# Kernel tuning notes

Measured on AMD Instinct MI355X. Metric: run time of the kernel, lower is better.

Reference implementation:

```python
import jax, jax.numpy as jnp
import numpy as np

B, S, D = 4, 2048, 1024
H = 16
HD = D // H  # head_dim = 64


def setup_inputs() -> dict:
    key = jax.random.key(0)
    ks = jax.random.split(key, 8)
    scale = 1.0 / np.sqrt(D)
    return {
        "X_Q": jax.random.normal(ks[0], (B, S, D), dtype=jnp.float32),
        "X_KV": jax.random.normal(ks[1], (B, S, D), dtype=jnp.float32),
        # q_proj: Linear(D, D), weights stored as (in, out)
        "q_w": jax.random.normal(ks[2], (D, D), dtype=jnp.float32) * scale,
        "q_b": jax.random.normal(ks[3], (D,), dtype=jnp.float32) * scale,
        # kv_proj: Linear(D, 2*D)
        "kv_w": jax.random.normal(ks[4], (D, 2 * D), dtype=jnp.float32) * scale,
        "kv_b": jax.random.normal(ks[5], (2 * D,), dtype=jnp.float32) * scale,
        # out_proj: Linear(D, D) (query_dim == input_dim)
        "out_w": jax.random.normal(ks[6], (D, D), dtype=jnp.float32) * scale,
        "out_b": jax.random.normal(ks[7], (D,), dtype=jnp.float32) * scale,
    }


def reference(X_Q, X_KV, q_w, q_b, kv_w, kv_b, out_w, out_b):
    # projections
    q = X_Q @ q_w + q_b                      # [b, s, D]
    kv = X_KV @ kv_w + kv_b                  # [b, l, 2D]
    k, v = jnp.split(kv, 2, axis=-1)         # each [b, l, D]

    def split_heads(t):
        b, m, _ = t.shape
        return t.reshape(b, m, H, HD).transpose(0, 2, 1, 3)  # [b, h, m, d]

    q, k, v = split_heads(q), split_heads(k), split_heads(v)

    # standard attention: full SxL scores (non-flash path)
    scores = jnp.einsum("bhsd,bhld->bhsl", q, k) / np.sqrt(HD)
    attn = jax.nn.softmax(scores, axis=-1)   # dropout_p = 0 -> identity
    out = jnp.einsum("bhsl,bhld->bhsd", attn, v)

    # merge heads: [b, h, s, d] -> [b, s, h*d]
    out = out.transpose(0, 2, 1, 3).reshape(B, S, D)
    return out @ out_w + out_b
```

## Files before the change

kernel.cpp:

```cpp
#include <hip/hip_runtime.h>
#include <hip/hip_bf16.h>
#include <math.h>

#define B_  4
#define S_  2048
#define D_  1024
#define H_  16
#define HD_ 64

typedef __bf16 bf16;
typedef __bf16 bf16x4 __attribute__((ext_vector_type(4)));
typedef __bf16 bf16x8 __attribute__((ext_vector_type(8)));
typedef float  floatx4 __attribute__((ext_vector_type(4)));
typedef unsigned short ushort8 __attribute__((ext_vector_type(8)));

#define QSCALE 0.18033688011112042f

__device__ __forceinline__ void async_load16(const bf16* g, bf16* l) {
  __builtin_amdgcn_global_load_lds(
      (const __attribute__((address_space(1))) void*)g,
      (__attribute__((address_space(3))) void*)l, 16, 0, 0);
}

__global__ __launch_bounds__(256) void cast_f32_bf16(
    const float* __restrict__ in, bf16* __restrict__ out, int n) {
  int i = (blockIdx.x * blockDim.x + threadIdx.x) * 4;
  if (i >= n) return;
  float4 v = *reinterpret_cast<const float4*>(in + i);
  bf16x4 o;
  o[0] = (bf16)v.x; o[1] = (bf16)v.y; o[2] = (bf16)v.z; o[3] = (bf16)v.w;
  *reinterpret_cast<bf16x4*>(out + i) = o;
}

__global__ __launch_bounds__(256) void transcast(
    const float* __restrict__ in, bf16* __restrict__ out, int K, int N) {
  __shared__ float tile[32][33];
  int k0 = blockIdx.y * 32, n0 = blockIdx.x * 32;
  int tx = threadIdx.x, ty = threadIdx.y;
  #pragma unroll
  for (int i = ty; i < 32; i += 8)
    tile[i][tx] = in[(size_t)(k0 + i) * N + n0 + tx];
  __syncthreads();
  #pragma unroll
  for (int i = ty; i < 32; i += 8)
    out[(size_t)(n0 + i) * K + k0 + tx] = (bf16)tile[tx][i];
}

template <int MODE>
__global__ __launch_bounds__(256) void gemm_bt(
    const bf16* __restrict__ A, const bf16* __restrict__ Bt,
    const float* __restrict__ bias, void* __restrict__ out,
    int M, int N, int K) {
  __shared__ bf16 As[128][64];
  __shared__ bf16 Bs[128][64];

  const int tid  = threadIdx.x;
  const int m0   = blockIdx.y * 128;
  const int n0   = blockIdx.x * 128;
  const int w    = tid >> 6;
  const int lane = tid & 63;
  const int lr   = lane & 15;
  const int lq   = lane >> 4;
  const int wm   = (w >> 1) * 64;
  const int wn   = (w & 1) * 64;

  const int srow = lane >> 3;
  const int sg   = (lane & 7) ^ srow;
  const bf16* aptr = A  + (size_t)(m0 + 32 * w + srow) * K + 8 * sg;
  const bf16* bptr = Bt + (size_t)(n0 + 32 * w + srow) * K + 8 * sg;

  floatx4 acc[4][4];
  #pragma unroll
  for (int i = 0; i < 4; i++)
    #pragma unroll
    for (int j = 0; j < 4; j++)
      acc[i][j] = floatx4{0.f, 0.f, 0.f, 0.f};

  for (int k0 = 0; k0 < K; k0 += 64) {
    __syncthreads();
    #pragma unroll
    for (int p = 0; p < 4; p++) {
      async_load16(aptr + (size_t)8 * p * K + k0, &As[32 * w + 8 * p][0]);
      async_load16(bptr + (size_t)8 * p * K + k0, &Bs[32 * w + 8 * p][0]);
    }
    __syncthreads();
    #pragma unroll
    for (int kc = 0; kc < 2; kc++) {
      const int sw = 8 * ((kc * 4 + lq) ^ (lr & 7));
      bf16x8 af[4], bfv[4];
      #pragma unroll
      for (int t = 0; t < 4; t++)
        af[t] = *reinterpret_cast<const bf16x8*>(&As[wm + 16 * t + lr][sw]);
      #pragma unroll
      for (int t = 0; t < 4; t++)
        bfv[t] = *reinterpret_cast<const bf16x8*>(&Bs[wn + 16 * t + lr][sw]);
      #pragma unroll
      for (int i = 0; i < 4; i++)
        #pragma unroll
        for (int j = 0; j < 4; j++)
          acc[i][j] = __builtin_amdgcn_mfma_f32_16x16x32_bf16(af[i], bfv[j], acc[i][j], 0, 0, 0);
    }
  }

  #pragma unroll
  for (int i = 0; i < 4; i++) {
    int row_base = m0 + wm + 16 * i + lq * 4;
    #pragma unroll
    for (int j = 0; j < 4; j++) {
      int col = n0 + wn + 16 * j + lr;
      float bv = bias[col];
      if (MODE == 2 && col >= 1024) {
        int b = row_base >> 11, s0 = row_base & 2047;
        int c = col - 1024, h = c >> 6, d = c & 63;
        bf16* Vt = (bf16*)out + (size_t)B_ * H_ * S_ * HD_;
        bf16x4 pk;
        #pragma unroll
        for (int r = 0; r < 4; r++) pk[r] = (bf16)(acc[i][j][r] + bv);
        *reinterpret_cast<bf16x4*>(
            &Vt[(((size_t)b * H_ + h) * HD_ + d) * S_ + s0]) = pk;
        continue;
      }
      #pragma unroll
      for (int r = 0; r < 4; r++) {
        int row = row_base + r;
        float v = acc[i][j][r] + bv;
        if (MODE == 0) {
          ((float*)out)[(size_t)row * N + col] = v;
        } else if (MODE == 1) {
          int b = row >> 11, s = row & 2047;
          int h = col >> 6, d = col & 63;
          ((bf16*)out)[(((size_t)b * H_ + h) * S_ + s) * HD_ + d] =
              (bf16)(v * QSCALE);
        } else {
          int b = row >> 11, s = row & 2047;
          int h = col >> 6, d = col & 63;
          ((bf16*)out)[(((size_t)b * H_ + h) * S_ + s) * HD_ + d] = (bf16)v;
        }
      }
    }
  }
}

__global__ __launch_bounds__(256, 4) void attn_kernel(
    const bf16* __restrict__ Q, const bf16* __restrict__ Kb,
    const bf16* __restrict__ Vt, bf16* __restrict__ out) {
  __shared__ bf16 smem[128 * 64 + 64 * 64 + 64 * 64];
  bf16 (*qs)[64]  = (bf16(*)[64])smem;
  bf16 (*ks)[64]  = (bf16(*)[64])(smem + 128 * 64);
  bf16 (*vts)[64] = (bf16(*)[64])(smem + 128 * 64 + 64 * 64);

  const int tid  = threadIdx.x;
  const int w    = tid >> 6;
  const int lane = tid & 63;
  const int lr   = lane & 15;
  const int lq   = lane >> 4;
  const int q0   = blockIdx.x * 128;
  const int bh   = blockIdx.y;
  const size_t base = (size_t)bh * S_ * HD_;

  bf16 (*pw)[64] = (bf16(*)[64])(smem + w * 2048);

  const int srow = lane >> 3;
  const int sg   = (lane & 7) ^ srow;

  const bf16* qsrc = Q  + base + (size_t)(q0 + 32 * w + srow) * HD_ + 8 * sg;
  #pragma unroll
  for (int p = 0; p < 4; p++)
    async_load16(qsrc + (size_t)8 * p * HD_, &qs[32 * w + 8 * p][0]);

  const bf16* kptr = Kb + base + (size_t)(16 * w + srow) * HD_ + 8 * sg;
  const bf16* vptr = Vt + base + (size_t)(16 * w + srow) * S_  + 8 * sg;

  #pragma unroll
  for (int p = 0; p < 2; p++) {
    async_load16(kptr + (size_t)8 * p * HD_, &ks[16 * w + 8 * p][0]);
    async_load16(vptr + (size_t)8 * p * S_,  &vts[16 * w + 8 * p][0]);
  }
  __syncthreads();

  const int sw0 = 8 * ((0 + lq) ^ (lr & 7));
  const int sw1 = 8 * ((4 + lq) ^ (lr & 7));
  bf16x8 bq[2][2];
  #pragma unroll
  for (int grp = 0; grp < 2; grp++) {
    bq[grp][0] = *reinterpret_cast<const bf16x8*>(&qs[32 * w + 16 * grp + lr][sw0]);
    bq[grp][1] = *reinterpret_cast<const bf16x8*>(&qs[32 * w + 16 * grp + lr][sw1]);
  }

  float l_i[2] = {0.f, 0.f};
  floatx4 o_acc[2][4];
  #pragma unroll
  for (int grp = 0; grp < 2; grp++)
    #pragma unroll
    for (int t = 0; t < 4; t++) o_acc[grp][t] = floatx4{0.f, 0.f, 0.f, 0.f};

  const int NIT = S_ / 64;
  for (int it = 0; it < NIT; it++) {
    floatx4 sc[2][4];
    #pragma unroll
    for (int grp = 0; grp < 2; grp++)
      #pragma unroll
      for (int t = 0; t < 4; t++) sc[grp][t] = floatx4{0.f, 0.f, 0.f, 0.f};
    #pragma unroll
    for (int kc = 0; kc < 2; kc++) {
      const int sw = kc ? sw1 : sw0;
      #pragma unroll
      for (int t = 0; t < 4; t++) {
        bf16x8 ak = *reinterpret_cast<const bf16x8*>(&ks[16 * t + lr][sw]);
        sc[0][t] = __builtin_amdgcn_mfma_f32_16x16x32_bf16(ak, bq[0][kc], sc[0][t], 0, 0, 0);
        sc[1][t] = __builtin_amdgcn_mfma_f32_16x16x32_bf16(ak, bq[1][kc], sc[1][t], 0, 0, 0);
      }
    }

    #pragma unroll
    for (int grp = 0; grp < 2; grp++) {
      float lsum = 0.f;
      #pragma unroll
      for (int t = 0; t < 4; t++) {
        bf16x4 pk;
        #pragma unroll
        for (int r = 0; r < 4; r++) {
          float p = __builtin_amdgcn_exp2f(sc[grp][t][r]);
          lsum += p;
          pk[r] = (bf16)p;
        }
        int col = 8 * ((2 * t + (lq >> 1)) ^ (lr & 7)) + 4 * (lq & 1);
        *reinterpret_cast<bf16x4*>(&pw[16 * grp + lr][col]) = pk;
      }
      l_i[grp] += lsum;
    }
    __builtin_amdgcn_wave_barrier();

    #pragma unroll
    for (int kc = 0; kc < 2; kc++) {
      const int sw = kc ? sw1 : sw0;
      bf16x8 bp0 = *reinterpret_cast<const bf16x8*>(&pw[lr][sw]);
      bf16x8 bp1 = *reinterpret_cast<const bf16x8*>(&pw[16 + lr][sw]);
      #pragma unroll
      for (int t = 0; t < 4; t++) {
        bf16x8 av = *reinterpret_cast<const bf16x8*>(&vts[16 * t + lr][sw]);
        o_acc[0][t] = __builtin_amdgcn_mfma_f32_16x16x32_bf16(av, bp0, o_acc[0][t], 0, 0, 0);
        o_acc[1][t] = __builtin_amdgcn_mfma_f32_16x16x32_bf16(av, bp1, o_acc[1][t], 0, 0, 0);
      }
    }

    if (it + 1 < NIT) {
      __syncthreads();
      const int l0n = (it + 1) * 64;
      #pragma unroll
      for (int p = 0; p < 2; p++) {
        async_load16(kptr + (size_t)(l0n + 8 * p) * HD_, &ks[16 * w + 8 * p][0]);
        async_load16(vptr + (size_t)8 * p * S_ + l0n,    &vts[16 * w + 8 * p][0]);
      }
      __syncthreads();
    }
  }

  #pragma unroll
  for (int grp = 0; grp < 2; grp++) {
    l_i[grp] += __shfl_xor(l_i[grp], 16, 64);
    l_i[grp] += __shfl_xor(l_i[grp], 32, 64);
  }

  const int b = bh >> 4, h = bh & 15;
  #pragma unroll
  for (int grp = 0; grp < 2; grp++) {
    const float inv = 1.0f / l_i[grp];
    const int qrow = q0 + 32 * w + 16 * grp + lr;
    bf16* orow = out + ((size_t)b * S_ + qrow) * D_ + h * HD_;
    #pragma unroll
    for (int t = 0; t < 4; t++) {
      bf16x4 pk;
      #pragma unroll
      for (int r = 0; r < 4; r++) pk[r] = (bf16)(o_acc[grp][t][r] * inv);
      *reinterpret_cast<bf16x4*>(&orow[16 * t + lq * 4]) = pk;
    }
  }
}

extern "C" void kernel_launch(void* const* d_in, const int* in_sizes, int n_in,
                              void* d_out, int out_size, void* d_ws, size_t ws_size,
                              hipStream_t stream) {
  const float* X_Q   = (const float*)d_in[0];
  const float* X_KV  = (const float*)d_in[1];
  const float* q_w   = (const float*)d_in[2];
  const float* q_b   = (const float*)d_in[3];
  const float* kv_w  = (const float*)d_in[4];
  const float* kv_b  = (const float*)d_in[5];
  const float* out_w = (const float*)d_in[6];
  const float* out_b = (const float*)d_in[7];
  float* out = (float*)d_out;

  char* ws = (char*)d_ws;
  const size_t MB = 1024 * 1024;
  bf16* Xq   = (bf16*)(ws + 0);
  bf16* Xkv  = (bf16*)(ws + 16 * MB);
  bf16* Qb   = (bf16*)(ws + 32 * MB);
  bf16* Kb   = (bf16*)(ws + 48 * MB);
  bf16* qwT  = (bf16*)(ws + 80 * MB);
  bf16* kvwT = (bf16*)(ws + 82 * MB);
  bf16* owT  = (bf16*)(ws + 86 * MB);
  bf16* Vt   = Kb + (size_t)B_ * H_ * S_ * HD_;
  bf16* attn = Xq;

  const int nX = B_ * S_ * D_;

  cast_f32_bf16<<<nX / 1024, 256, 0, stream>>>(X_Q, Xq, nX);
  cast_f32_bf16<<<nX / 1024, 256, 0, stream>>>(X_KV, Xkv, nX);
  transcast<<<dim3(32, 32), dim3(32, 8), 0, stream>>>(q_w, qwT, 1024, 1024);
  transcast<<<dim3(64, 32), dim3(32, 8), 0, stream>>>(kv_w, kvwT, 1024, 2048);
  transcast<<<dim3(32, 32), dim3(32, 8), 0, stream>>>(out_w, owT, 1024, 1024);

  gemm_bt<1><<<dim3(8, 64), 256, 0, stream>>>(Xq, qwT, q_b, Qb, 8192, 1024, 1024);
  gemm_bt<2><<<dim3(16, 64), 256, 0, stream>>>(Xkv, kvwT, kv_b, Kb, 8192, 2048, 1024);
  attn_kernel<<<dim3(16, 64), 256, 0, stream>>>(Qb, Kb, Vt, attn);
  gemm_bt<0><<<dim3(8, 64), 256, 0, stream>>>(attn, owT, out_b, out, 8192, 1024, 1024);
}
```

Baseline: 336.9 us.

## Double-buffer K/V in attention, widen query tile, and merge prep kernels

```diff
diff --git a/kernel.cpp b/kernel.cpp
--- a/kernel.cpp
+++ b/kernel.cpp
@@ -22,28 +22,41 @@
       (__attribute__((address_space(3))) void*)l, 16, 0, 0);
 }
 
-__global__ __launch_bounds__(256) void cast_f32_bf16(
-    const float* __restrict__ in, bf16* __restrict__ out, int n) {
-  int i = (blockIdx.x * blockDim.x + threadIdx.x) * 4;
-  if (i >= n) return;
+__global__ __launch_bounds__(256) void cast_both(
+    const float* __restrict__ ina, bf16* __restrict__ outa,
+    const float* __restrict__ inb, bf16* __restrict__ outb) {
+  int bid = blockIdx.x;
+  const float* in;
+  bf16* out;
+  int i;
+  if (bid < 8192) { in = ina; out = outa; i = (bid * 256 + threadIdx.x) * 4; }
+  else            { in = inb; out = outb; i = ((bid - 8192) * 256 + threadIdx.x) * 4; }
   float4 v = *reinterpret_cast<const float4*>(in + i);
   bf16x4 o;
   o[0] = (bf16)v.x; o[1] = (bf16)v.y; o[2] = (bf16)v.z; o[3] = (bf16)v.w;
   *reinterpret_cast<bf16x4*>(out + i) = o;
 }
 
-__global__ __launch_bounds__(256) void transcast(
-    const float* __restrict__ in, bf16* __restrict__ out, int K, int N) {
+__global__ __launch_bounds__(256) void transcast_all(
+    const float* __restrict__ qw, bf16* __restrict__ qwT,
+    const float* __restrict__ kvw, bf16* __restrict__ kvwT,
+    const float* __restrict__ ow, bf16* __restrict__ owT) {
   __shared__ float tile[32][33];
-  int k0 = blockIdx.y * 32, n0 = blockIdx.x * 32;
-  int tx = threadIdx.x, ty = threadIdx.y;
+  int bid = blockIdx.x;
+  const float* in; bf16* out; int N, lb;
+  if (bid < 1024)      { in = qw;  out = qwT;  N = 1024; lb = bid; }
+  else if (bid < 3072) { in = kvw; out = kvwT; N = 2048; lb = bid - 1024; }
+  else                 { in = ow;  out = owT;  N = 1024; lb = bid - 3072; }
+  int nx = N >> 5;
+  int n0 = (lb % nx) * 32, k0 = (lb / nx) * 32;
+  int tx = threadIdx.x & 31, ty = threadIdx.x >> 5;
   #pragma unroll
   for (int i = ty; i < 32; i += 8)
     tile[i][tx] = in[(size_t)(k0 + i) * N + n0 + tx];
   __syncthreads();
   #pragma unroll
   for (int i = ty; i < 32; i += 8)
-    out[(size_t)(n0 + i) * K + k0 + tx] = (bf16)tile[tx][i];
+    out[(size_t)(n0 + i) * 1024 + k0 + tx] = (bf16)tile[tx][i];
 }
 
 template <int MODE>
@@ -141,138 +154,135 @@
   }
 }
 
-__global__ __launch_bounds__(256, 4) void attn_kernel(
+__global__ __launch_bounds__(256, 2) void attn_kernel(
     const bf16* __restrict__ Q, const bf16* __restrict__ Kb,
     const bf16* __restrict__ Vt, bf16* __restrict__ out) {
-  __shared__ bf16 smem[128 * 64 + 64 * 64 + 64 * 64];
-  bf16 (*qs)[64]  = (bf16(*)[64])smem;
-  bf16 (*ks)[64]  = (bf16(*)[64])(smem + 128 * 64);
-  bf16 (*vts)[64] = (bf16(*)[64])(smem + 128 * 64 + 64 * 64);
+  __shared__ bf16 smem[32768];
 
   const int tid  = threadIdx.x;
   const int w    = tid >> 6;
   const int lane = tid & 63;
   const int lr   = lane & 15;
   const int lq   = lane >> 4;
-  const int q0   = blockIdx.x * 128;
+  const int q0   = blockIdx.x * 256;
   const int bh   = blockIdx.y;
   const size_t base = (size_t)bh * S_ * HD_;
 
-  bf16 (*pw)[64] = (bf16(*)[64])(smem + w * 2048);
+  bf16* pw = smem + 16384 + w * 4096;
 
   const int srow = lane >> 3;
   const int sg   = (lane & 7) ^ srow;
 
-  const bf16* qsrc = Q  + base + (size_t)(q0 + 32 * w + srow) * HD_ + 8 * sg;
-  #pragma unroll
-  for (int p = 0; p < 4; p++)
-    async_load16(qsrc + (size_t)8 * p * HD_, &qs[32 * w + 8 * p][0]);
-
   const bf16* kptr = Kb + base + (size_t)(16 * w + srow) * HD_ + 8 * sg;
   const bf16* vptr = Vt + base + (size_t)(16 * w + srow) * S_  + 8 * sg;
 
   #pragma unroll
   for (int p = 0; p < 2; p++) {
-    async_load16(kptr + (size_t)8 * p * HD_, &ks[16 * w + 8 * p][0]);
-    async_load16(vptr + (size_t)8 * p * S_,  &vts[16 * w + 8 * p][0]);
-  }
-  __syncthreads();
+    async_load16(kptr + (size_t)8 * p * HD_, smem + (16 * w + 8 * p) * 64);
+    async_load16(vptr + (size_t)8 * p * S_,  smem + 4096 + (16 * w + 8 * p) * 64);
+  }
+
+  bf16x8 bq[4][2];
+  #pragma unroll
+  for (int g = 0; g < 4; g++) {
+    const bf16* qrow = Q + base + (size_t)(q0 + 64 * w + 16 * g + lr) * HD_;
+    bq[g][0] = *reinterpret_cast<const bf16x8*>(qrow + lq * 8);
+    bq[g][1] = *reinterpret_cast<const bf16x8*>(qrow + 32 + lq * 8);
+  }
 
   const int sw0 = 8 * ((0 + lq) ^ (lr & 7));
   const int sw1 = 8 * ((4 + lq) ^ (lr & 7));
-  bf16x8 bq[2][2];
-  #pragma unroll
-  for (int grp = 0; grp < 2; grp++) {
-    bq[grp][0] = *reinterpret_cast<const bf16x8*>(&qs[32 * w + 16 * grp + lr][sw0]);
-    bq[grp][1] = *reinterpret_cast<const bf16x8*>(&qs[32 * w + 16 * grp + lr][sw1]);
-  }
-
-  float l_i[2] = {0.f, 0.f};
-  floatx4 o_acc[2][4];
-  #pragma unroll
-  for (int grp = 0; grp < 2; grp++)
-    #pragma unroll
-    for (int t = 0; t < 4; t++) o_acc[grp][t] = floatx4{0.f, 0.f, 0.f, 0.f};
+  const int pcolbase = 4 * (lq & 1);
+  const int pswz = lr & 7;
+
+  float l_i[4] = {0.f, 0.f, 0.f, 0.f};
+  floatx4 o_acc[4][4];
+  #pragma unroll
+  for (int g = 0; g < 4; g++)
+    #pragma unroll
+    for (int t = 0; t < 4; t++) o_acc[g][t] = floatx4{0.f, 0.f, 0.f, 0.f};
+
+  __syncthreads();
 
   const int NIT = S_ / 64;
   for (int it = 0; it < NIT; it++) {
-    floatx4 sc[2][4];
-    #pragma unroll
-    for (int grp = 0; grp < 2; grp++)
-      #pragma unroll
-      for (int t = 0; t < 4; t++) sc[grp][t] = floatx4{0.f, 0.f, 0.f, 0.f};
-    #pragma unroll
-    for (int kc = 0; kc < 2; kc++) {
-      const int sw = kc ? sw1 : sw0;
-      #pragma unroll
-      for (int t = 0; t < 4; t++) {
-        bf16x8 ak = *reinterpret_cast<const bf16x8*>(&ks[16 * t + lr][sw]);
-        sc[0][t] = __builtin_amdgcn_mfma_f32_16x16x32_bf16(ak, bq[0][kc], sc[0][t], 0, 0, 0);
-        sc[1][t] = __builtin_amdgcn_mfma_f32_16x16x32_bf16(ak, bq[1][kc], sc[1][t], 0, 0, 0);
-      }
-    }
-
-    #pragma unroll
-    for (int grp = 0; grp < 2; grp++) {
-      float lsum = 0.f;
-      #pragma unroll
-      for (int t = 0; t < 4; t++) {
+    bf16* ks  = smem + (it & 1) * 8192;
+    bf16* vts = ks + 4096;
+
+    if (it + 1 < NIT) {
+      bf16* ksn = smem + ((it + 1) & 1) * 8192;
+      const int l0n = (it + 1) * 64;
+      #pragma unroll
+      for (int p = 0; p < 2; p++) {
+        async_load16(kptr + (size_t)(l0n + 8 * p) * HD_, ksn + (16 * w + 8 * p) * 64);
+        async_load16(vptr + (size_t)8 * p * S_ + l0n,    ksn + 4096 + (16 * w + 8 * p) * 64);
+      }
+    }
+
+    #pragma unroll
+    for (int t = 0; t < 4; t++) {
+      bf16x8 ak0 = *reinterpret_cast<const bf16x8*>(ks + (16 * t + lr) * 64 + sw0);
+      bf16x8 ak1 = *reinterpret_cast<const bf16x8*>(ks + (16 * t + lr) * 64 + sw1);
+      floatx4 sc[4];
+      #pragma unroll
+      for (int g = 0; g < 4; g++) {
+        sc[g] = __builtin_amdgcn_mfma_f32_16x16x32_bf16(ak0, bq[g][0],
+                    floatx4{0.f, 0.f, 0.f, 0.f}, 0, 0, 0);
+        sc[g] = __builtin_amdgcn_mfma_f32_16x16x32_bf16(ak1, bq[g][1], sc[g], 0, 0, 0);
+      }
+      const int pcol = 8 * ((2 * t + (lq >> 1)) ^ pswz) + pcolbase;
+      #pragma unroll
+      for (int g = 0; g < 4; g++) {
         bf16x4 pk;
+        float lsum = 0.f;
         #pragma unroll
         for (int r = 0; r < 4; r++) {
-          float p = __builtin_amdgcn_exp2f(sc[grp][t][r]);
+          float p = __builtin_amdgcn_exp2f(sc[g][r]);
           lsum += p;
           pk[r] = (bf16)p;
         }
-        int col = 8 * ((2 * t + (lq >> 1)) ^ (lr & 7)) + 4 * (lq & 1);
-        *reinterpret_cast<bf16x4*>(&pw[16 * grp + lr][col]) = pk;
-      }
-      l_i[grp] += lsum;
+        l_i[g] += lsum;
+        *reinterpret_cast<bf16x4*>(&pw[(16 * g + lr) * 64 + pcol]) = pk;
+      }
     }
     __builtin_amdgcn_wave_barrier();
 
     #pragma unroll
     for (int kc = 0; kc < 2; kc++) {
       const int sw = kc ? sw1 : sw0;
-      bf16x8 bp0 = *reinterpret_cast<const bf16x8*>(&pw[lr][sw]);
-      bf16x8 bp1 = *reinterpret_cast<const bf16x8*>(&pw[16 + lr][sw]);
+      bf16x8 bp[4];
+      #pragma unroll
+      for (int g = 0; g < 4; g++)
+        bp[g] = *reinterpret_cast<const bf16x8*>(&pw[(16 * g + lr) * 64 + sw]);
       #pragma unroll
       for (int t = 0; t < 4; t++) {
-        bf16x8 av = *reinterpret_cast<const bf16x8*>(&vts[16 * t + lr][sw]);
-        o_acc[0][t] = __builtin_amdgcn_mfma_f32_16x16x32_bf16(av, bp0, o_acc[0][t], 0, 0, 0);
-        o_acc[1][t] = __builtin_amdgcn_mfma_f32_16x16x32_bf16(av, bp1, o_acc[1][t], 0, 0, 0);
-      }
-    }
-
-    if (it + 1 < NIT) {
-      __syncthreads();
-      const int l0n = (it + 1) * 64;
-      #pragma unroll
-      for (int p = 0; p < 2; p++) {
-        async_load16(kptr + (size_t)(l0n + 8 * p) * HD_, &ks[16 * w + 8 * p][0]);
-        async_load16(vptr + (size_t)8 * p * S_ + l0n,    &vts[16 * w + 8 * p][0]);
-      }
-      __syncthreads();
-    }
-  }
-
-  #pragma unroll
-  for (int grp = 0; grp < 2; grp++) {
-    l_i[grp] += __shfl_xor(l_i[grp], 16, 64);
-    l_i[grp] += __shfl_xor(l_i[grp], 32, 64);
+        bf16x8 av = *reinterpret_cast<const bf16x8*>(vts + (16 * t + lr) * 64 + sw);
+        #pragma unroll
+        for (int g = 0; g < 4; g++)
+          o_acc[g][t] = __builtin_amdgcn_mfma_f32_16x16x32_bf16(av, bp[g], o_acc[g][t], 0, 0, 0);
+      }
+    }
+
+    __syncthreads();
+  }
+
+  #pragma unroll
+  for (int g = 0; g < 4; g++) {
+    l_i[g] += __shfl_xor(l_i[g], 16, 64);
+    l_i[g] += __shfl_xor(l_i[g], 32, 64);
   }
 
   const int b = bh >> 4, h = bh & 15;
   #pragma unroll
-  for (int grp = 0; grp < 2; grp++) {
-    const float inv = 1.0f / l_i[grp];
-    const int qrow = q0 + 32 * w + 16 * grp + lr;
+  for (int g = 0; g < 4; g++) {
+    const float inv = 1.0f / l_i[g];
+    const int qrow = q0 + 64 * w + 16 * g + lr;
     bf16* orow = out + ((size_t)b * S_ + qrow) * D_ + h * HD_;
     #pragma unroll
     for (int t = 0; t < 4; t++) {
       bf16x4 pk;
       #pragma unroll
-      for (int r = 0; r < 4; r++) pk[r] = (bf16)(o_acc[grp][t][r] * inv);
+      for (int r = 0; r < 4; r++) pk[r] = (bf16)(o_acc[g][t][r] * inv);
       *reinterpret_cast<bf16x4*>(&orow[16 * t + lq * 4]) = pk;
     }
   }
@@ -303,16 +313,11 @@
   bf16* Vt   = Kb + (size_t)B_ * H_ * S_ * HD_;
   bf16* attn = Xq;
 
-  const int nX = B_ * S_ * D_;
-
-  cast_f32_bf16<<<nX / 1024, 256, 0, stream>>>(X_Q, Xq, nX);
-  cast_f32_bf16<<<nX / 1024, 256, 0, stream>>>(X_KV, Xkv, nX);
-  transcast<<<dim3(32, 32), dim3(32, 8), 0, stream>>>(q_w, qwT, 1024, 1024);
-  transcast<<<dim3(64, 32), dim3(32, 8), 0, stream>>>(kv_w, kvwT, 1024, 2048);
-  transcast<<<dim3(32, 32), dim3(32, 8), 0, stream>>>(out_w, owT, 1024, 1024);
+  cast_both<<<16384, 256, 0, stream>>>(X_Q, Xq, X_KV, Xkv);
+  transcast_all<<<4096, 256, 0, stream>>>(q_w, qwT, kv_w, kvwT, out_w, owT);
 
   gemm_bt<1><<<dim3(8, 64), 256, 0, stream>>>(Xq, qwT, q_b, Qb, 8192, 1024, 1024);
   gemm_bt<2><<<dim3(16, 64), 256, 0, stream>>>(Xkv, kvwT, kv_b, Kb, 8192, 2048, 1024);
-  attn_kernel<<<dim3(16, 64), 256, 0, stream>>>(Qb, Kb, Vt, attn);
+  attn_kernel<<<dim3(8, 64), 256, 0, stream>>>(Qb, Kb, Vt, attn);
   gemm_bt<0><<<dim3(8, 64), 256, 0, stream>>>(attn, owT, out_b, out, 8192, 1024, 1024);
 }
```

New measurement: 314.5 us. -6.6%, faster.
